# Kernel tuning notes

Hardware: AMD Instinct MI355X
Metric: run time of the kernel (lower is better)

The kernel has to match this reference:

```python
import jax, jax.numpy as jnp
import numpy as np

EPS = 1e-5
K = 20
NH = 16
SLOPE = 0.2

def leaky(x):
    return jnp.where(x >= 0, x, SLOPE * x)

def bn(x, g, b, axes):
    # training-mode batch norm (biased variance), channel axis = 1
    m = x.mean(axes, keepdims=True)
    v = x.var(axes, keepdims=True)
    shp = [1] * x.ndim
    shp[1] = -1
    return (x - m) / jnp.sqrt(v + EPS) * g.reshape(shp) + b.reshape(shp)

def efr(x, idx, w, k):
    # x: [B, C, N]; idx: flat global gather indices [B*N*k]; w: [C_out, 2C+1]
    B, C, N = x.shape
    xt = x.transpose(0, 2, 1).reshape(B * N, C)
    feature = xt[idx].reshape(B, N, k, C)            # gathered neighbors
    xc = xt.reshape(B, N, 1, C)
    fmean = feature.mean(-1, keepdims=True)          # [B,N,k,1]
    f = jnp.concatenate([feature - xc, fmean, jnp.broadcast_to(xc, feature.shape)], axis=3)
    return jnp.einsum('bnkc,oc->bonk', f, w)         # 1x1 conv -> [B,C_out,N,k]


def setup_inputs() -> dict:
    key = jax.random.key(0)
    ks = jax.random.split(key, 24)
    B, N = 8, 4096
    IN_CH, FEAT_CH, OUT_CH = 6, 64, 64
    d = {}
    d['points'] = jax.random.normal(ks[0], (B, IN_CH // 2, N), dtype=jnp.float32)
    d['feat'] = jax.random.normal(ks[1], (B, FEAT_CH // 2, N), dtype=jnp.float32)
    d['idx'] = jax.random.randint(ks[2], (B * N * K,), 0, B * N)
    s = 0.1
    d['w_efr_p'] = jax.random.normal(ks[3], (IN_CH, IN_CH + 1), dtype=jnp.float32) * s
    d['w_efr_f'] = jax.random.normal(ks[4], (FEAT_CH, FEAT_CH + 1), dtype=jnp.float32) * s
    d['w_q'] = jax.random.normal(ks[5], (FEAT_CH, FEAT_CH // 2), dtype=jnp.float32) * s
    d['g_q'] = jnp.ones((FEAT_CH,), jnp.float32)
    d['b_q'] = jnp.zeros((FEAT_CH,), jnp.float32)
    d['w_pos1'] = jax.random.normal(ks[6], (IN_CH, IN_CH // 2), dtype=jnp.float32) * s
    d['g_pos1'] = jnp.ones((IN_CH,), jnp.float32)
    d['b_pos1'] = jnp.zeros((IN_CH,), jnp.float32)
    d['w_pos2'] = jax.random.normal(ks[7], (FEAT_CH, IN_CH), dtype=jnp.float32) * s
    d['w_attn'] = jax.random.normal(ks[8], (NH * IN_CH, FEAT_CH), dtype=jnp.float32) * s
    d['g1'] = jnp.ones((NH,), jnp.float32)
    d['b1'] = jnp.zeros((NH,), jnp.float32)
    d['w_lin'] = jax.random.normal(ks[9], (OUT_CH, NH), dtype=jnp.float32) * s
    d['g_lin'] = jnp.ones((OUT_CH,), jnp.float32)
    d['b_lin'] = jnp.zeros((OUT_CH,), jnp.float32)
    d['w_res'] = jax.random.normal(ks[10], (OUT_CH, FEAT_CH), dtype=jnp.float32) * s
    d['g_res'] = jnp.ones((OUT_CH,), jnp.float32)
    d['b_res'] = jnp.zeros((OUT_CH,), jnp.float32)
    return d


def reference(points, feat, idx, w_efr_p, w_efr_f, w_q, g_q, b_q,
              w_pos1, g_pos1, b_pos1, w_pos2, w_attn, g1, b1,
              w_lin, g_lin, b_lin, w_res, g_res, b_res):
    B, _, N = points.shape
    knn_points = efr(points, idx, w_efr_p, K)   # [B,6,N,K]
    knn_feat = efr(feat, idx, w_efr_f, K)       # [B,64,N,K]
    x_q = leaky(bn(jnp.einsum('bcn,oc->bon', feat, w_q), g_q, b_q, (0, 2)))
    pos = leaky(bn(jnp.einsum('bcn,oc->bon', points, w_pos1), g_pos1, b_pos1, (0, 2)))
    pos = pos[:, :, :, None] - knn_points       # [B,6,N,K]
    pos = jnp.einsum('bcnk,oc->bonk', pos, w_pos2)  # [B,64,N,K]
    attn = x_q[:, :, :, None] - knn_feat + pos
    attn = jax.nn.softmax(attn / float(np.sqrt(knn_feat.shape[1])), axis=-1)
    attn = jnp.einsum('bcnk,oc->bonk', attn, w_attn)  # [B,NH*6,N,K]
    attn5 = attn.transpose(0, 2, 3, 1).reshape(B, N, K, NH, -1)  # [B,N,K,NH,6]
    y = jnp.einsum('bnkhc,bcnk->bhnk', attn5, knn_points)        # [B,NH,N,K]
    y = leaky(bn(y, g1, b1, (0, 2, 3)))
    y = bn(jnp.einsum('bcnk,oc->bonk', y, w_lin), g_lin, b_lin, (0, 2, 3))
    res = bn(jnp.einsum('bcnk,oc->bonk', knn_feat, w_res), g_res, b_res, (0, 2, 3))
    y = leaky(y + res)
    return y.max(axis=-1)                        # [B,64,N]
```

## Files before the change

kernel.cpp:

```cpp
#include <hip/hip_runtime.h>

#define KNN 20
#define NN 4096
#define NPTS 32768
#define PPW 8

using short8 = __attribute__((ext_vector_type(8))) short;
using f32x4v = __attribute__((ext_vector_type(4))) float;
using uint4v = __attribute__((ext_vector_type(4))) unsigned int;

__device__ __forceinline__ float lrelu(float x){ return x >= 0.f ? x : 0.2f*x; }
__device__ __forceinline__ unsigned short f2b(float x){
    union { float f; unsigned u; } v; v.f = x;
    unsigned r = v.u + 0x7FFFu + ((v.u >> 16) & 1u);
    return (unsigned short)(r >> 16);
}
__device__ __forceinline__ float b2f(unsigned h){
    union { unsigned u; float f; } v; v.u = h << 16; return v.f;
}
#define WSYNC() do { asm volatile("s_waitcnt lgkmcnt(0)" ::: "memory"); __builtin_amdgcn_sched_barrier(0); } while(0)

__device__ __forceinline__ int fslot(int fragi, int klocal, int gp){
    return fragi*1024 + (((klocal) + ((gp)<<4)) ^ ((gp)*5))*16;
}

__global__ void kprep(const float* __restrict__ weff, const float* __restrict__ wattn,
                      const float* __restrict__ wres, const float* __restrict__ wl,
                      unsigned short* __restrict__ packW, float* __restrict__ wdiff,
                      float* __restrict__ w32t, float* __restrict__ wrb,
                      float* __restrict__ rww)
{
    __shared__ float sres[4096];
    __shared__ float sweff[4160];
    __shared__ float scomb[2048];
    int t = threadIdx.x;
    for (int m=t; m<4096; m+=256) sres[m] = wres[m];
    for (int m=t; m<4160; m+=256) sweff[m] = weff[m];
    __syncthreads();
    for (int q=t;q<2048;q+=256){
        int c=q>>5, j=q&31;
        wdiff[q] = sweff[c*65+33+j]-sweff[c*65+j];
    }
    if (t<64) w32t[t] = sweff[t*65+32];
    for (int q=t;q<2048;q+=256){
        int o=q>>5, j=q&31;
        float a=0.f, b=0.f;
        for (int c=0;c<64;c++){
            float wr = sres[o*64+c];
            a += wr*sweff[c*65+j];
            b += wr*(sweff[c*65+33+j]-sweff[c*65+j]);
        }
        scomb[q]=a; wrb[q]=b;
    }
    if (t<64){
        float a=0.f;
        for (int c=0;c<64;c++) a += sres[t*64+c]*sweff[c*65+32];
        rww[t]=a;
    }
    __syncthreads();
    for (int q = t; q < 1536; q += 256){
        int f = q >> 6, l = q & 63;
        #pragma unroll
        for (int j=0;j<8;j++){
            int koff, n; float v;
            if (f < 4){ n = f*16 + (l&15); koff = 0;
                int k = koff + (j>=4?16:0) + 4*(l>>4) + (j&3);
                v = sweff[n*65 + k];
            } else if (f < 16){ int ff=f-4; n = (ff>>1)*16 + (l&15); koff = (ff&1)*32;
                int k = koff + (j>=4?16:0) + 4*(l>>4) + (j&3);
                v = wattn[n*64 + k];
            } else { int ff=f-16; n = (ff>>1)*16 + (l&15); koff = (ff&1)*32;
                int k = koff + (j>=4?16:0) + 4*(l>>4) + (j&3);
                v = sres[n*64 + k];
            }
            packW[(size_t)(f*64+l)*8 + j] = f2b(v);
        }
    }
    for (int q=t;q<512;q+=256){
        int f=q>>6, l=q&63;
        int nt = f&3; bool iswl = f>=4;
        #pragma unroll
        for (int j=0;j<8;j++){
            int kdim = (j>=4?16:0)+4*(l>>4)+(j&3);
            float v;
            if (!iswl) v = scomb[(nt*16+(l&15))*32 + kdim];
            else v = (kdim<16) ? wl[(nt*16+(l&15))*16 + kdim] : 0.f;
            packW[(size_t)((24+f)*64+l)*8+j] = f2b(v);
        }
    }
}

__global__ void __launch_bounds__(256) k0_prep(
    const float* __restrict__ pts, const float* __restrict__ feat,
    const float* __restrict__ wq, const float* __restrict__ wpos1,
    const float* __restrict__ wefp, const float* __restrict__ wdiff,
    const float* __restrict__ wrb,
    unsigned short* __restrict__ ft16, float* __restrict__ pt4,
    unsigned short* __restrict__ qp16, float* __restrict__ pp,
    unsigned short* __restrict__ base16, float* __restrict__ bpp,
    unsigned short* __restrict__ rb16,
    float* __restrict__ qsum, float* __restrict__ qsq,
    float* __restrict__ psum, float* __restrict__ psq)
{
    __shared__ float swq[2048];
    __shared__ float swd[2048];
    __shared__ float swr[2048];
    __shared__ float red[4][64], red2[4][64];
    int tid = threadIdx.x;
    for (int m=tid;m<2048;m+=256){ swq[m]=wq[m]; swd[m]=wdiff[m]; swr[m]=wrb[m]; }
    __syncthreads();
    int r = blockIdx.x*256 + tid;
    int b = r >> 12, n = r & 4095;
    float p0 = pts[((size_t)b*3+0)*NN+n];
    float p1 = pts[((size_t)b*3+1)*NN+n];
    float p2 = pts[((size_t)b*3+2)*NN+n];
    float pm = (p0+p1+p2)*(1.f/3.f);
    *(float4*)(pt4 + (size_t)r*4) = make_float4(p0,p1,p2,pm);
    float f[32];
    #pragma unroll
    for (int c=0;c<32;c++) f[c] = feat[((size_t)b*32+c)*NN+n];
    #pragma unroll
    for (int c=0;c<32;c+=2){
        unsigned pk = (unsigned)f2b(f[c]) | ((unsigned)f2b(f[c+1])<<16);
        *(unsigned*)(ft16 + (size_t)r*32 + c) = pk;
    }
    float q[64];
    for (int o=0;o<64;o++){
        float a=0.f;
        #pragma unroll
        for (int c=0;c<32;c++) a += swq[o*32+c]*f[c];
        q[o]=a;
    }
    for (int o=0;o<64;o+=2){
        unsigned pk = (unsigned)f2b(q[o]) | ((unsigned)f2b(q[o+1])<<16);
        *(unsigned*)(qp16 + (size_t)r*64 + o) = pk;
    }
    int lane = tid & 63, wvv = tid>>6;
    for (int o=0;o<64;o++){
        float s=q[o], s2=q[o]*q[o];
        for (int d=1; d<64; d<<=1){ s += __shfl_xor(s,d); s2 += __shfl_xor(s2,d); }
        if (lane==0){ red[wvv][o]=s; red2[wvv][o]=s2; }
    }
    __syncthreads();
    if (tid<64){
        atomicAdd(qsum+tid, red[0][tid]+red[1][tid]+red[2][tid]+red[3][tid]);
        atomicAdd(qsq+tid, red2[0][tid]+red2[1][tid]+red2[2][tid]+red2[3][tid]);
    }
    for (int o=0;o<64;o++){
        float a=0.f;
        #pragma unroll
        for (int c=0;c<32;c++) a += swd[o*32+c]*f[c];
        q[o]=a;
    }
    for (int o=0;o<64;o+=2){
        unsigned pk = (unsigned)f2b(q[o]) | ((unsigned)f2b(q[o+1])<<16);
        *(unsigned*)(base16 + (size_t)r*64 + o) = pk;
    }
    for (int o=0;o<64;o++){
        float a=0.f;
        #pragma unroll
        for (int c=0;c<32;c++) a += swr[o*32+c]*f[c];
        q[o]=a;
    }
    for (int o=0;o<64;o+=2){
        unsigned pk = (unsigned)f2b(q[o]) | ((unsigned)f2b(q[o+1])<<16);
        *(unsigned*)(rb16 + (size_t)r*64 + o) = pk;
    }
    float pr[8];
    #pragma unroll
    for (int o=0;o<6;o++) pr[o] = wpos1[o*3]*p0 + wpos1[o*3+1]*p1 + wpos1[o*3+2]*p2;
    pr[6]=0.f; pr[7]=0.f;
    *(float4*)(pp+(size_t)r*8)   = make_float4(pr[0],pr[1],pr[2],pr[3]);
    *(float4*)(pp+(size_t)r*8+4) = make_float4(pr[4],pr[5],pr[6],pr[7]);
    __syncthreads();
    for (int o=0;o<6;o++){
        float s=pr[o], s2=pr[o]*pr[o];
        for (int d=1;d<64;d<<=1){ s += __shfl_xor(s,d); s2 += __shfl_xor(s2,d); }
        if (lane==0){ red[wvv][o]=s; red2[wvv][o]=s2; }
    }
    __syncthreads();
    if (tid<6){
        atomicAdd(psum+tid, red[0][tid]+red[1][tid]+red[2][tid]+red[3][tid]);
        atomicAdd(psq+tid, red2[0][tid]+red2[1][tid]+red2[2][tid]+red2[3][tid]);
    }
    #pragma unroll
    for (int j=0;j<6;j++)
        bpp[(size_t)r*8+j] = p0*(wefp[j*7+4]-wefp[j*7]) + p1*(wefp[j*7+5]-wefp[j*7+1])
                           + p2*(wefp[j*7+6]-wefp[j*7+2]);
    bpp[(size_t)r*8+6]=0.f; bpp[(size_t)r*8+7]=0.f;
}

__global__ void k1_paramsA(
    const float* __restrict__ qsum, const float* __restrict__ qsq,
    const float* __restrict__ psum, const float* __restrict__ psq,
    const float* __restrict__ gq, const float* __restrict__ bq,
    const float* __restrict__ gp, const float* __restrict__ bp,
    float* __restrict__ bnq_a, float* __restrict__ bnq_c,
    float* __restrict__ bnp_a, float* __restrict__ bnp_c)
{
    int t = threadIdx.x;
    const float inv = 1.f/32768.f;
    if (t < 64){
        float m = qsum[t]*inv; float v = qsq[t]*inv - m*m;
        float a = gq[t]*rsqrtf(v + 1e-5f);
        bnq_a[t] = a; bnq_c[t] = bq[t] - m*a;
    }
    if (t < 6){
        float m = psum[t]*inv; float v = psq[t]*inv - m*m;
        float a = gp[t]*rsqrtf(v + 1e-5f);
        bnp_a[t] = a; bnp_c[t] = bp[t] - m*a;
    }
}

#define ARENA 10240
#define R1    0
#define R2    4096
#define SFM   8192
#define SSKP  8320
#define SIDX  8960
#define YST   9600

__global__ void __launch_bounds__(256, 3) k2_main(
    const unsigned short* __restrict__ ft16, const float* __restrict__ pt4,
    const unsigned short* __restrict__ qp16, const float* __restrict__ pp,
    const unsigned short* __restrict__ base16, const float* __restrict__ bpp,
    const int* __restrict__ idx,
    const float* __restrict__ wefp, const float* __restrict__ wpos2,
    const unsigned short* __restrict__ packW, const float* __restrict__ w32t,
    const float* __restrict__ bnq_a, const float* __restrict__ bnq_c,
    const float* __restrict__ bnp_a, const float* __restrict__ bnp_c,
    unsigned short* __restrict__ yv,
    float* __restrict__ yslot, float* __restrict__ rslot)
{
    __shared__ __align__(16) char smem_[4*ARENA];
    const int tid = threadIdx.x;
    const int l = tid & 63, wv = tid >> 6;
    const int lo = l & 15, g = l >> 4;
    char* S = smem_ + wv*ARENA;
    const int srd = (l ^ (g*5))*16;

    float w2r[4][6], w32r[4], bnqa[4], bnqc[4];
    #pragma unroll
    for (int nt=0;nt<4;nt++){
        #pragma unroll
        for (int j=0;j<6;j++) w2r[nt][j] = wpos2[(nt*16+lo)*6+j];
        w32r[nt] = w32t[nt*16+lo];
        bnqa[nt] = bnq_a[nt*16+lo];
        bnqc[nt] = bnq_c[nt*16+lo];
    }
    float bnpa[6], bnpc[6];
    #pragma unroll
    for (int j=0;j<6;j++){ bnpa[j]=bnp_a[j]; bnpc[j]=bnp_c[j]; }

    float ysum=0.f, ysq=0.f;
    float racc[4]={0.f,0.f,0.f,0.f}, rsqa[4]={0.f,0.f,0.f,0.f};

    const int rbase = blockIdx.x*(4*PPW) + wv*PPW;

    *(int*)(S+SIDX+l*4)        = idx[(size_t)rbase*KNN + l];
    *(int*)(S+SIDX+(64+l)*4)   = idx[(size_t)rbase*KNN + 64 + l];
    if (l < 32) *(int*)(S+SIDX+(128+l)*4) = idx[(size_t)rbase*KNN + 128 + l];
    WSYNC();

    for (int pi=0; pi<PPW; pi++){
        const size_t r = (size_t)(rbase + pi);
        float xqv[4], basev[4], sp[6];
        {
            int sb = pi*KNN*4;
            int i0 = *(const int*)(S+SIDX+sb+(l>>3)*4);
            int i1 = *(const int*)(S+SIDX+sb+(8+(l>>3))*4);
            uint2 ng0 = *(const uint2*)(ft16 + (size_t)i0*32 + (l&7)*4);
            uint2 ng1 = *(const uint2*)(ft16 + (size_t)i1*32 + (l&7)*4);
            uint2 ng2 = make_uint2(0u,0u);
            if (l < 32){
                int i2 = *(const int*)(S+SIDX+sb+(16+(l>>3))*4);
                ng2 = *(const uint2*)(ft16 + (size_t)i2*32 + (l&7)*4);
            }
            float4 ngp4 = make_float4(0,0,0,0);
            if (l < KNN){
                int ip = *(const int*)(S+SIDX+sb+l*4);
                ngp4 = *(const float4*)(pt4 + (size_t)ip*4);
            }
            float nbppr[6];
            if (l < KNN){
                #pragma unroll
                for (int j=0;j<6;j++) nbppr[j] = bpp[r*8+j];
            }
            float s0 = b2f(ng0.x&0xffffu)+b2f(ng0.x>>16)+b2f(ng0.y&0xffffu)+b2f(ng0.y>>16);
            float s1 = b2f(ng1.x&0xffffu)+b2f(ng1.x>>16)+b2f(ng1.y&0xffffu)+b2f(ng1.y>>16);
            float s2 = b2f(ng2.x&0xffffu)+b2f(ng2.x>>16)+b2f(ng2.y&0xffffu)+b2f(ng2.y>>16);
            s0 += __shfl_xor(s0,1); s0 += __shfl_xor(s0,2); s0 += __shfl_xor(s0,4);
            s1 += __shfl_xor(s1,1); s1 += __shfl_xor(s1,2); s1 += __shfl_xor(s1,4);
            s2 += __shfl_xor(s2,1); s2 += __shfl_xor(s2,2); s2 += __shfl_xor(s2,4);
            if ((l&7)==0){
                *(float*)(S+SFM+(l>>3)*4) = s0*(1.f/32.f);
                *(float*)(S+SFM+(8+(l>>3))*4) = s1*(1.f/32.f);
                if (l < 32) *(float*)(S+SFM+(16+(l>>3))*4) = s2*(1.f/32.f);
            }
            {
                int kk = l>>3, gp_ = l&3, jb = ((l>>2)&1)*8;
                *(uint2*)(S + R1 + fslot(0, kk, gp_) + jb) = ng0;
                *(uint2*)(S + R1 + fslot(0, 8+kk, gp_) + jb) = ng1;
                if (l < 32) *(uint2*)(S + R1 + fslot(1, kk, gp_) + jb) = ng2;
            }
            if (l < KNN){
                #pragma unroll
                for (int j=0;j<6;j++){
                    float v = nbppr[j] + wefp[j*7]*ngp4.x + wefp[j*7+1]*ngp4.y
                            + wefp[j*7+2]*ngp4.z + wefp[j*7+3]*ngp4.w;
                    *(float*)(S+SSKP+(l*8+j)*4) = v;
                }
            }
            #pragma unroll
            for (int nt=0;nt<4;nt++){
                xqv[nt] = lrelu(bnqa[nt]*b2f(qp16[r*64 + nt*16+lo]) + bnqc[nt]);
                basev[nt] = b2f(base16[r*64 + nt*16+lo]);
            }
            #pragma unroll
            for (int j=0;j<6;j++) sp[j] = lrelu(bnpa[j]*pp[r*8+j] + bnpc[j]);
            WSYNC();
        }

        f32x4v C1[2][4];
        #pragma unroll
        for (int mt=0;mt<2;mt++)
            #pragma unroll
            for (int nt=0;nt<4;nt++)
                #pragma unroll
                for (int i=0;i<4;i++) C1[mt][nt][i] = 0.f;
        short8 Af0 = *(const short8*)(S + R1 + 0*1024 + srd);
        short8 Af1 = *(const short8*)(S + R1 + 1*1024 + srd);
        #pragma unroll
        for (int nt=0;nt<4;nt++){
            short8 Bf = *(const short8*)(packW + (size_t)(nt*64 + l)*8);
            C1[0][nt] = __builtin_amdgcn_mfma_f32_16x16x32_bf16(Af0, Bf, C1[0][nt], 0, 0, 0);
            C1[1][nt] = __builtin_amdgcn_mfma_f32_16x16x32_bf16(Af1, Bf, C1[1][nt], 0, 0, 0);
        }
        #pragma unroll
        for (int mt=0;mt<2;mt++){
            #pragma unroll
            for (int i=0;i<4;i++){
                int k = mt*16 + g*4 + i;
                bool valid = (k < KNN);
                int kk = valid ? k : 0;
                float fmk = *(const float*)(S+SFM+kk*4);
                float sk[6];
                #pragma unroll
                for (int j=0;j<6;j++) sk[j] = *(const float*)(S+SSKP+(kk*8+j)*4);
                #pragma unroll
                for (int nt=0;nt<4;nt++){
                    float kf = C1[mt][nt][i] + basev[nt] + w32r[nt]*fmk;
                    if (valid){
                        int fa = fslot(mt*2+(nt>>1), g*4+i, lo>>2) + ((nt&1)*4 + (lo&3))*2;
                        *(unsigned short*)(S + R2 + fa) = f2b(kf);
                    }
                    float pos = 0.f;
                    #pragma unroll
                    for (int j=0;j<6;j++) pos += (sp[j]-sk[j])*w2r[nt][j];
                    C1[mt][nt][i] = valid ? (xqv[nt] - kf + pos)*0.125f : -1e30f;
                }
            }
        }
        #pragma unroll
        for (int nt=0;nt<4;nt++){
            float mx = -1e30f;
            #pragma unroll
            for (int mt=0;mt<2;mt++)
                #pragma unroll
                for (int i=0;i<4;i++) mx = fmaxf(mx, C1[mt][nt][i]);
            mx = fmaxf(mx, __shfl_xor(mx,16));
            mx = fmaxf(mx, __shfl_xor(mx,32));
            float sm = 0.f;
            #pragma unroll
            for (int mt=0;mt<2;mt++)
                #pragma unroll
                for (int i=0;i<4;i++){ float e = __expf(C1[mt][nt][i]-mx); C1[mt][nt][i]=e; sm += e; }
            sm += __shfl_xor(sm,16);
            sm += __shfl_xor(sm,32);
            float inv = 1.f/sm;
            #pragma unroll
            for (int mt=0;mt<2;mt++)
                #pragma unroll
                for (int i=0;i<4;i++){
                    int k = mt*16 + g*4 + i;
                    if (k < KNN){
                        int fa = fslot(mt*2+(nt>>1), g*4+i, lo>>2) + ((nt&1)*4 + (lo&3))*2;
                        *(unsigned short*)(S + R1 + fa) = f2b(C1[mt][nt][i]*inv);
                    }
                }
        }
        WSYNC();
        short8 Ak[2][2], Aa[2][2];
        #pragma unroll
        for (int mt=0;mt<2;mt++)
            #pragma unroll
            for (int s=0;s<2;s++){
                Ak[mt][s] = *(const short8*)(S + R2 + (mt*2+s)*1024 + srd);
                Aa[mt][s] = *(const short8*)(S + R1 + (mt*2+s)*1024 + srd);
            }
        f32x4v C3[2][4];
        #pragma unroll
        for (int mt=0;mt<2;mt++)
            #pragma unroll
            for (int nt=0;nt<4;nt++)
                #pragma unroll
                for (int i=0;i<4;i++) C3[mt][nt][i] = 0.f;
        #pragma unroll
        for (int nt=0;nt<4;nt++){
            #pragma unroll
            for (int s=0;s<2;s++){
                short8 Bf = *(const short8*)(packW + (size_t)((16+nt*2+s)*64 + l)*8);
                #pragma unroll
                for (int mt=0;mt<2;mt++)
                    C3[mt][nt] = __builtin_amdgcn_mfma_f32_16x16x32_bf16(Ak[mt][s], Bf, C3[mt][nt], 0, 0, 0);
            }
        }
        #pragma unroll
        for (int mt=0;mt<2;mt++)
            #pragma unroll
            for (int i=0;i<4;i++){
                int k = mt*16 + g*4 + i;
                if (k < KNN){
                    #pragma unroll
                    for (int nt=0;nt<4;nt++){
                        float v = C3[mt][nt][i];
                        racc[nt] += v; rsqa[nt] += v*v;
                    }
                }
            }
        f32x4v C2[2][6];
        #pragma unroll
        for (int mt=0;mt<2;mt++)
            #pragma unroll
            for (int nt=0;nt<6;nt++)
                #pragma unroll
                for (int i=0;i<4;i++) C2[mt][nt][i] = 0.f;
        #pragma unroll
        for (int nt=0;nt<6;nt++){
            #pragma unroll
            for (int s=0;s<2;s++){
                short8 Bf = *(const short8*)(packW + (size_t)((4+nt*2+s)*64 + l)*8);
                #pragma unroll
                for (int mt=0;mt<2;mt++)
                    C2[mt][nt] = __builtin_amdgcn_mfma_f32_16x16x32_bf16(Aa[mt][s], Bf, C2[mt][nt], 0, 0, 0);
            }
        }
        #pragma unroll
        for (int mt=0;mt<2;mt++)
            #pragma unroll
            for (int nt=0;nt<6;nt++)
                #pragma unroll
                for (int i=0;i<4;i++){
                    int k = mt*16 + g*4 + i;
                    if (k < KNN)
                        *(unsigned short*)(S + R2 + k*200 + (nt*16+lo)*2) = f2b(C2[mt][nt][i]);
                }
        WSYNC();
        #pragma unroll
        for (int it=0; it<5; it++){
            int kq = it*4 + g;
            const char* row = S + R2 + kq*200 + lo*12;
            unsigned d0 = *(const unsigned*)(row);
            unsigned d1 = *(const unsigned*)(row+4);
            unsigned d2 = *(const unsigned*)(row+8);
            float yval = b2f(d0&0xffffu) * (*(const float*)(S+SSKP+(kq*8+0)*4))
                       + b2f(d0>>16)    * (*(const float*)(S+SSKP+(kq*8+1)*4))
                       + b2f(d1&0xffffu)* (*(const float*)(S+SSKP+(kq*8+2)*4))
                       + b2f(d1>>16)    * (*(const float*)(S+SSKP+(kq*8+3)*4))
                       + b2f(d2&0xffffu)* (*(const float*)(S+SSKP+(kq*8+4)*4))
                       + b2f(d2>>16)    * (*(const float*)(S+SSKP+(kq*8+5)*4));
            *(unsigned short*)(S + YST + kq*32 + lo*2) = f2b(yval);
            ysum += yval; ysq += yval*yval;
        }
        WSYNC();
        if (l < 40){
            uint4v v = *(const uint4v*)(S + YST + l*16);
            *(uint4v*)((char*)yv + r*640 + l*16) = v;
        }
    }
    ysum += __shfl_xor(ysum,16); ysum += __shfl_xor(ysum,32);
    ysq  += __shfl_xor(ysq,16);  ysq  += __shfl_xor(ysq,32);
    #pragma unroll
    for (int nt=0;nt<4;nt++){
        racc[nt] += __shfl_xor(racc[nt],16); racc[nt] += __shfl_xor(racc[nt],32);
        rsqa[nt] += __shfl_xor(rsqa[nt],16); rsqa[nt] += __shfl_xor(rsqa[nt],32);
    }
    int slot = (blockIdx.x*4 + wv) & 63;
    if (l < 16){
        atomicAdd(yslot + slot*32 + l, ysum);
        #pragma unroll
        for (int nt=0;nt<4;nt++) atomicAdd(rslot + slot*128 + nt*16 + l, racc[nt]);
    } else if (l < 32){
        atomicAdd(yslot + slot*32 + 16 + lo, ysq);
        #pragma unroll
        for (int nt=0;nt<4;nt++) atomicAdd(rslot + slot*128 + 64 + nt*16 + lo, rsqa[nt]);
    }
}

__global__ void k3_paramsB(
    const float* __restrict__ yslot, const float* __restrict__ rslot,
    const float* __restrict__ g1, const float* __restrict__ b1,
    const float* __restrict__ gr, const float* __restrict__ br,
    float* __restrict__ bn1_a, float* __restrict__ bn1_c,
    float* __restrict__ bnr_a, float* __restrict__ bnr_c)
{
    __shared__ float sy[32];
    __shared__ float sr[128];
    int t = threadIdx.x;
    float s1 = 0.f;
    if (t < 32){ for (int i=0;i<64;i++) s1 += yslot[(size_t)i*32+t]; }
    float s2 = 0.f;
    for (int i=0;i<64;i++) s2 += rslot[(size_t)i*128+t];
    if (t < 32) sy[t] = s1;
    sr[t] = s2;
    __syncthreads();
    const float inv = 1.f/655360.f;
    if (t < 16){
        float m = sy[t]*inv; float v = sy[16+t]*inv - m*m;
        float a = g1[t]*rsqrtf(v + 1e-5f);
        bn1_a[t] = a; bn1_c[t] = b1[t] - m*a;
    }
    if (t < 64){
        float m = sr[t]*inv; float v = sr[64+t]*inv - m*m;
        float a = gr[t]*rsqrtf(v + 1e-5f);
        bnr_a[t] = a; bnr_c[t] = br[t] - m*a;
    }
}

__global__ void __launch_bounds__(256) k4_linstats(
    const unsigned short* __restrict__ yv,
    const float* __restrict__ bn1_a, const float* __restrict__ bn1_c,
    float* __restrict__ Mslot, float* __restrict__ Sslot)
{
    __shared__ __align__(16) char lds[4*1024];
    const int tid = threadIdx.x, l = tid & 63, wvv = tid >> 6;
    const int lo = l & 15, g = l >> 4;
    char* L = lds + wvv*1024;
    const int h0 = (l&1)*8;
    float a8[8], c8[8];
    #pragma unroll
    for (int j=0;j<8;j++){ a8[j]=bn1_a[h0+j]; c8[j]=bn1_c[h0+j]; }
    short8 ones;
    #pragma unroll
    for (int j=0;j<8;j++) ones[j] = (short)0x3F80;
    f32x4v Macc, Sacc;
    #pragma unroll
    for (int i=0;i<4;i++){ Macc[i]=0.f; Sacc[i]=0.f; }
    const int waveid = blockIdx.x*4 + wvv;
    for (int it=0; it<5; it++){
        size_t s0 = ((size_t)waveid*5 + it)*32;
        uint4 v = *(const uint4*)(yv + s0*16 + l*8);
        unsigned short e0 = v.x&0xffffu, e1 = v.x>>16, e2 = v.y&0xffffu, e3 = v.y>>16;
        unsigned short e4 = v.z&0xffffu, e5 = v.z>>16, e6 = v.w&0xffffu, e7 = v.w>>16;
        float y0 = lrelu(a8[0]*b2f(e0)+c8[0]), y1 = lrelu(a8[1]*b2f(e1)+c8[1]);
        float y2_ = lrelu(a8[2]*b2f(e2)+c8[2]), y3 = lrelu(a8[3]*b2f(e3)+c8[3]);
        float y4 = lrelu(a8[4]*b2f(e4)+c8[4]), y5 = lrelu(a8[5]*b2f(e5)+c8[5]);
        float y6 = lrelu(a8[6]*b2f(e6)+c8[6]), y7 = lrelu(a8[7]*b2f(e7)+c8[7]);
        uint4 o;
        o.x = (unsigned)f2b(y0) | ((unsigned)f2b(y1)<<16);
        o.y = (unsigned)f2b(y2_)| ((unsigned)f2b(y3)<<16);
        o.z = (unsigned)f2b(y4) | ((unsigned)f2b(y5)<<16);
        o.w = (unsigned)f2b(y6) | ((unsigned)f2b(y7)<<16);
        *(uint4*)(L + l*16) = o;
        WSYNC();
        short8 Af;
        #pragma unroll
        for (int j=0;j<8;j++){
            int s = 4*g + (j&3) + ((j>=4)?16:0);
            Af[j] = *(const short*)(L + s*32 + lo*2);
        }
        WSYNC();
        Macc = __builtin_amdgcn_mfma_f32_16x16x32_bf16(Af, Af, Macc, 0, 0, 0);
        Sacc = __builtin_amdgcn_mfma_f32_16x16x32_bf16(ones, Af, Sacc, 0, 0, 0);
    }
    float* Ms = Mslot + (size_t)(waveid&15)*256;
    #pragma unroll
    for (int i=0;i<4;i++) atomicAdd(Ms + (g*4+i)*16 + lo, Macc[i]);
    if (l < 16) atomicAdd(Sslot + (size_t)(waveid&15)*16 + lo, Sacc[0]);
}

__global__ void k5_paramsC(
    const float* __restrict__ Mslot, const float* __restrict__ Sslot,
    const float* __restrict__ wl,
    const float* __restrict__ gl, const float* __restrict__ bl,
    float* __restrict__ bnl_a, float* __restrict__ bnl_c)
{
    __shared__ float Ms[256], Ss[16];
    int t = threadIdx.x;
    float m = 0.f;
    for (int i=0;i<16;i++) m += Mslot[(size_t)i*256+t];
    Ms[t] = m;
    if (t < 16){
        float s = 0.f;
        for (int i=0;i<16;i++) s += Sslot[(size_t)i*16+t];
        Ss[t] = s;
    }
    __syncthreads();
    if (t < 64){
        float w[16];
        #pragma unroll
        for (int h=0;h<16;h++) w[h] = wl[t*16+h];
        float lsum = 0.f;
        #pragma unroll
        for (int h=0;h<16;h++) lsum += w[h]*Ss[h];
        float lsq = 0.f;
        for (int h1=0;h1<16;h1++){
            float acc = 0.f;
            #pragma unroll
            for (int h2=0;h2<16;h2++) acc += Ms[h1*16+h2]*w[h2];
            lsq += w[h1]*acc;
        }
        const float inv = 1.f/655360.f;
        float mean = lsum*inv; float var = lsq*inv - mean*mean;
        float a = gl[t]*rsqrtf(var + 1e-5f);
        bnl_a[t] = a; bnl_c[t] = bl[t] - mean*a;
    }
}

#define ARENA6 2848
#define SFM6 2048
#define SIDX6 2176

__global__ void __launch_bounds__(256) k6_final(
    const unsigned short* __restrict__ ft16, const unsigned short* __restrict__ yv,
    const int* __restrict__ idx, const unsigned short* __restrict__ rb16,
    const unsigned short* __restrict__ packW, const float* __restrict__ rww,
    const float* __restrict__ bn1_a, const float* __restrict__ bn1_c,
    const float* __restrict__ bnl_a, const float* __restrict__ bnl_c,
    const float* __restrict__ bnr_a, const float* __restrict__ bnr_c,
    float* __restrict__ out)
{
    __shared__ __align__(16) char smem_[4*ARENA6];
    __shared__ float sval[64*36];
    const int tid = threadIdx.x;
    const int l = tid & 63, wv = tid >> 6;
    const int lo = l & 15, g = l >> 4;
    char* S = smem_ + wv*ARENA6;
    const int srd = (l ^ (g*5))*16;

    short8 Bc[4], Bl[4];
    #pragma unroll
    for (int nt=0;nt<4;nt++){
        Bc[nt] = *(const short8*)(packW + (size_t)((24+nt)*64+l)*8);
        Bl[nt] = *(const short8*)(packW + (size_t)((28+nt)*64+l)*8);
    }
    float4 b1a = *(const float4*)(bn1_a + 4*g);
    float4 b1c = *(const float4*)(bn1_c + 4*g);
    float la[4], lc[4], ra[4], rc[4], rwv[4];
    #pragma unroll
    for (int nt=0;nt<4;nt++){
        int o = nt*16+lo;
        la[nt]=bnl_a[o]; lc[nt]=bnl_c[o]; ra[nt]=bnr_a[o]; rc[nt]=bnr_c[o]; rwv[nt]=rww[o];
    }
    const int rbase = blockIdx.x*32 + wv*8;
    *(int*)(S+SIDX6+l*4)      = idx[(size_t)rbase*KNN + l];
    *(int*)(S+SIDX6+(64+l)*4) = idx[(size_t)rbase*KNN + 64 + l];
    if (l < 32) *(int*)(S+SIDX6+(128+l)*4) = idx[(size_t)rbase*KNN + 128 + l];
    WSYNC();

    for (int pi=0; pi<8; pi++){
        size_t rr = (size_t)(rbase + pi);
        short8 AlyA, AlyB; float rbv[4];
        {
            int sb = pi*KNN*4;
            int i0 = *(const int*)(S+SIDX6+sb+(l>>3)*4);
            int i1 = *(const int*)(S+SIDX6+sb+(8+(l>>3))*4);
            uint2 ng0 = *(const uint2*)(ft16 + (size_t)i0*32 + (l&7)*4);
            uint2 ng1 = *(const uint2*)(ft16 + (size_t)i1*32 + (l&7)*4);
            uint2 ng2 = make_uint2(0u,0u);
            if (l < 32){
                int i2 = *(const int*)(S+SIDX6+sb+(16+(l>>3))*4);
                ng2 = *(const uint2*)(ft16 + (size_t)i2*32 + (l&7)*4);
            }
            uint2 ylo_ = *(const uint2*)(yv + rr*320 + (l&15)*16 + g*4);
            uint2 yhi_ = make_uint2(0u,0u);
            if (lo < 4) yhi_ = *(const uint2*)(yv + rr*320 + (16+(l&15))*16 + g*4);
            unsigned short rbr[4];
            #pragma unroll
            for (int nt=0;nt<4;nt++) rbr[nt] = rb16[rr*64 + nt*16+lo];

            float s0 = b2f(ng0.x&0xffffu)+b2f(ng0.x>>16)+b2f(ng0.y&0xffffu)+b2f(ng0.y>>16);
            float s1 = b2f(ng1.x&0xffffu)+b2f(ng1.x>>16)+b2f(ng1.y&0xffffu)+b2f(ng1.y>>16);
            float s2 = b2f(ng2.x&0xffffu)+b2f(ng2.x>>16)+b2f(ng2.y&0xffffu)+b2f(ng2.y>>16);
            s0 += __shfl_xor(s0,1); s0 += __shfl_xor(s0,2); s0 += __shfl_xor(s0,4);
            s1 += __shfl_xor(s1,1); s1 += __shfl_xor(s1,2); s1 += __shfl_xor(s1,4);
            s2 += __shfl_xor(s2,1); s2 += __shfl_xor(s2,2); s2 += __shfl_xor(s2,4);
            if ((l&7)==0){
                *(float*)(S+SFM6+(l>>3)*4) = s0*(1.f/32.f);
                *(float*)(S+SFM6+(8+(l>>3))*4) = s1*(1.f/32.f);
                if (l < 32) *(float*)(S+SFM6+(16+(l>>3))*4) = s2*(1.f/32.f);
            }
            {
                int kk = l>>3, gp_ = l&3, jb = ((l>>2)&1)*8;
                *(uint2*)(S + fslot(0, kk, gp_) + jb) = ng0;
                *(uint2*)(S + fslot(0, 8+kk, gp_) + jb) = ng1;
                if (l < 32) *(uint2*)(S + fslot(1, kk, gp_) + jb) = ng2;
            }
            float t0 = lrelu(b1a.x*b2f(ylo_.x&0xffffu)+b1c.x);
            float t1 = lrelu(b1a.y*b2f(ylo_.x>>16)+b1c.y);
            float t2 = lrelu(b1a.z*b2f(ylo_.y&0xffffu)+b1c.z);
            float t3 = lrelu(b1a.w*b2f(ylo_.y>>16)+b1c.w);
            AlyA[0]=(short)f2b(t0); AlyA[1]=(short)f2b(t1); AlyA[2]=(short)f2b(t2); AlyA[3]=(short)f2b(t3);
            AlyA[4]=0; AlyA[5]=0; AlyA[6]=0; AlyA[7]=0;
            t0 = lrelu(b1a.x*b2f(yhi_.x&0xffffu)+b1c.x);
            t1 = lrelu(b1a.y*b2f(yhi_.x>>16)+b1c.y);
            t2 = lrelu(b1a.z*b2f(yhi_.y&0xffffu)+b1c.z);
            t3 = lrelu(b1a.w*b2f(yhi_.y>>16)+b1c.w);
            AlyB[0]=(short)f2b(t0); AlyB[1]=(short)f2b(t1); AlyB[2]=(short)f2b(t2); AlyB[3]=(short)f2b(t3);
            AlyB[4]=0; AlyB[5]=0; AlyB[6]=0; AlyB[7]=0;
            #pragma unroll
            for (int nt=0;nt<4;nt++) rbv[nt] = b2f(rbr[nt]);
            WSYNC();
        }

        short8 Af0 = *(const short8*)(S + 0*1024 + srd);
        short8 Af1 = *(const short8*)(S + 1*1024 + srd);
        f32x4v Crv[2][4], Clv[2][4];
        #pragma unroll
        for (int mt=0;mt<2;mt++)
            #pragma unroll
            for (int nt=0;nt<4;nt++)
                #pragma unroll
                for (int i=0;i<4;i++){ Crv[mt][nt][i]=0.f; Clv[mt][nt][i]=0.f; }
        #pragma unroll
        for (int nt=0;nt<4;nt++){
            Crv[0][nt] = __builtin_amdgcn_mfma_f32_16x16x32_bf16(Af0, Bc[nt], Crv[0][nt], 0, 0, 0);
            Crv[1][nt] = __builtin_amdgcn_mfma_f32_16x16x32_bf16(Af1, Bc[nt], Crv[1][nt], 0, 0, 0);
            Clv[0][nt] = __builtin_amdgcn_mfma_f32_16x16x32_bf16(AlyA, Bl[nt], Clv[0][nt], 0, 0, 0);
            Clv[1][nt] = __builtin_amdgcn_mfma_f32_16x16x32_bf16(AlyB, Bl[nt], Clv[1][nt], 0, 0, 0);
        }
        float vmax[4] = {-1e30f,-1e30f,-1e30f,-1e30f};
        #pragma unroll
        for (int mt=0;mt<2;mt++)
            #pragma unroll
            for (int i=0;i<4;i++){
                int k = mt*16 + g*4 + i;
                if (k < KNN){
                    float fmk = *(const float*)(S+SFM6+k*4);
                    #pragma unroll
                    for (int nt=0;nt<4;nt++){
                        float rv = Crv[mt][nt][i] + rbv[nt] + rwv[nt]*fmk;
                        float lv = Clv[mt][nt][i];
                        float val = lrelu(la[nt]*lv + lc[nt] + ra[nt]*rv + rc[nt]);
                        vmax[nt] = fmaxf(vmax[nt], val);
                    }
                }
            }
        #pragma unroll
        for (int nt=0;nt<4;nt++){
            vmax[nt] = fmaxf(vmax[nt], __shfl_xor(vmax[nt],16));
            vmax[nt] = fmaxf(vmax[nt], __shfl_xor(vmax[nt],32));
        }
        if (l < 16){
            #pragma unroll
            for (int nt=0;nt<4;nt++)
                sval[(nt*16+lo)*36 + wv*8 + pi] = vmax[nt];
        }
        WSYNC();
    }
    __syncthreads();
    {
        int o = tid >> 2, seg = tid & 3;
        float4 v0 = *(const float4*)(sval + o*36 + seg*8);
        float4 v1 = *(const float4*)(sval + o*36 + seg*8 + 4);
        size_t base = ((size_t)(blockIdx.x>>7)*64 + o)*NN + (blockIdx.x&127)*32 + seg*8;
        *(float4*)(out + base) = v0;
        *(float4*)(out + base + 4) = v1;
    }
}

extern "C" void kernel_launch(void* const* d_in, const int* in_sizes, int n_in,
                              void* d_out, int out_size, void* d_ws, size_t ws_size,
                              hipStream_t stream)
{
    const float* pts   = (const float*)d_in[0];
    const float* feat  = (const float*)d_in[1];
    const int*   idx   = (const int*)d_in[2];
    const float* wefp  = (const float*)d_in[3];
    const float* weff  = (const float*)d_in[4];
    const float* wq    = (const float*)d_in[5];
    const float* gq    = (const float*)d_in[6];
    const float* bq    = (const float*)d_in[7];
    const float* wpos1 = (const float*)d_in[8];
    const float* gp    = (const float*)d_in[9];
    const float* bp    = (const float*)d_in[10];
    const float* wpos2 = (const float*)d_in[11];
    const float* wattn = (const float*)d_in[12];
    const float* g1    = (const float*)d_in[13];
    const float* b1    = (const float*)d_in[14];
    const float* wl    = (const float*)d_in[15];
    const float* gl    = (const float*)d_in[16];
    const float* bl    = (const float*)d_in[17];
    const float* wres  = (const float*)d_in[18];
    const float* gr    = (const float*)d_in[19];
    const float* br    = (const float*)d_in[20];
    float* out = (float*)d_out;

    char* ws = (char*)d_ws;
    size_t o_ft16 = 0;
    size_t o_pt4  = o_ft16 + (size_t)NPTS*64;
    size_t o_qp16 = o_pt4  + (size_t)NPTS*16;
    size_t o_pp   = o_qp16 + (size_t)NPTS*128;
    size_t o_b16  = o_pp   + (size_t)NPTS*32;
    size_t o_bpp  = o_b16  + (size_t)NPTS*128;
    size_t o_rb16 = o_bpp  + (size_t)NPTS*32;
    size_t o_packW= o_rb16 + (size_t)NPTS*128;
    size_t o_wdiff= o_packW + 32*512*2;
    size_t o_wrb  = o_wdiff + 2048*4;
    size_t o_rw   = o_wrb   + 2048*4;
    size_t o_w32  = o_rw    + 64*4;
    size_t o_st   = o_w32   + 64*4;
    size_t o_qsum  = o_st;
    size_t o_qsq   = o_qsum + 64*4;
    size_t o_psum  = o_qsq  + 64*4;
    size_t o_psq   = o_psum + 8*4;
    size_t o_yslot = o_psq  + 8*4;
    size_t o_rslot = o_yslot + (size_t)64*32*4;
    size_t o_mslot = o_rslot + (size_t)64*128*4;
    size_t o_sslot = o_mslot + (size_t)16*256*4;
    size_t zero_bytes = (o_sslot + (size_t)16*16*4) - o_st;
    size_t o_par   = o_st + zero_bytes;
    size_t o_bnq_a = o_par;
    size_t o_bnq_c = o_bnq_a + 64*4;
    size_t o_bnp_a = o_bnq_c + 64*4;
    size_t o_bnp_c = o_bnp_a + 8*4;
    size_t o_bn1_a = o_bnp_c + 8*4;
    size_t o_bn1_c = o_bn1_a + 16*4;
    size_t o_bnl_a = o_bn1_c + 16*4;
    size_t o_bnl_c = o_bnl_a + 64*4;
    size_t o_bnr_a = o_bnl_c + 64*4;
    size_t o_bnr_c = o_bnr_a + 64*4;
    size_t o_yv = (o_bnr_c + 64*4 + 255) & ~(size_t)255;

    unsigned short* ft16 = (unsigned short*)(ws + o_ft16);
    float* pt4  = (float*)(ws + o_pt4);
    unsigned short* qp16 = (unsigned short*)(ws + o_qp16);
    float* ppb  = (float*)(ws + o_pp);
    unsigned short* b16p = (unsigned short*)(ws + o_b16);
    float* bppb = (float*)(ws + o_bpp);
    unsigned short* rb16 = (unsigned short*)(ws + o_rb16);
    unsigned short* packW = (unsigned short*)(ws + o_packW);
    float* wdiff= (float*)(ws + o_wdiff);
    float* wrb  = (float*)(ws + o_wrb);
    float* rww  = (float*)(ws + o_rw);
    float* w32t = (float*)(ws + o_w32);
    float* qsum = (float*)(ws + o_qsum);
    float* qsq  = (float*)(ws + o_qsq);
    float* psum = (float*)(ws + o_psum);
    float* psq  = (float*)(ws + o_psq);
    float* yslot= (float*)(ws + o_yslot);
    float* rslot= (float*)(ws + o_rslot);
    float* Mslot= (float*)(ws + o_mslot);
    float* Sslot= (float*)(ws + o_sslot);
    float* bnq_a= (float*)(ws + o_bnq_a);
    float* bnq_c= (float*)(ws + o_bnq_c);
    float* bnp_a= (float*)(ws + o_bnp_a);
    float* bnp_c= (float*)(ws + o_bnp_c);
    float* bn1_a= (float*)(ws + o_bn1_a);
    float* bn1_c= (float*)(ws + o_bn1_c);
    float* bnl_a= (float*)(ws + o_bnl_a);
    float* bnl_c= (float*)(ws + o_bnl_c);
    float* bnr_a= (float*)(ws + o_bnr_a);
    float* bnr_c= (float*)(ws + o_bnr_c);
    unsigned short* yvp = (unsigned short*)(ws + o_yv);

    (void)hipMemsetAsync(ws + o_st, 0, zero_bytes, stream);

    kprep<<<1, 256, 0, stream>>>(weff, wattn, wres, wl, packW, wdiff, w32t, wrb, rww);
    k0_prep<<<128, 256, 0, stream>>>(pts, feat, wq, wpos1, wefp, wdiff, wrb,
                                     ft16, pt4, qp16, ppb, b16p, bppb, rb16,
                                     qsum, qsq, psum, psq);
    k1_paramsA<<<1, 64, 0, stream>>>(qsum, qsq, psum, psq, gq, bq, gp, bp,
                                     bnq_a, bnq_c, bnp_a, bnp_c);
    k2_main<<<NPTS/(4*PPW), 256, 0, stream>>>(ft16, pt4, qp16, ppb, b16p, bppb, idx,
                                     wefp, wpos2, packW, w32t,
                                     bnq_a, bnq_c, bnp_a, bnp_c,
                                     yvp, yslot, rslot);
    k3_paramsB<<<1, 128, 0, stream>>>(yslot, rslot, g1, b1, gr, br,
                                      bn1_a, bn1_c, bnr_a, bnr_c);
    k4_linstats<<<1024, 256, 0, stream>>>(yvp, bn1_a, bn1_c, Mslot, Sslot);
    k5_paramsC<<<1, 256, 0, stream>>>(Mslot, Sslot, wl, gl, bl, bnl_a, bnl_c);
    k6_final<<<1024, 256, 0, stream>>>(ft16, yvp, idx, rb16, packW, rww,
                                       bn1_a, bn1_c, bnl_a, bnl_c, bnr_a, bnr_c, out);
}
```

Measured before the change: 480.5 us.

## Interleave bf16 features and points into 128-byte gather records; read idx directly

Packs each point's bf16 features (64 bytes) and its float4 point/mean into a single 128-byte record, so a neighbour's feature and coordinate gathers fall in the same cache line. The per-wave LDS staging of neighbour indices is removed from both k2_main and k6_final; indices are now read straight from global memory. This shrinks the LDS arenas, which could allow higher occupancy. The cost is extra global idx loads per point and a doubled stride for feature records.

After: 508.6 us. +5.9%, slower.

```diff
diff --git a/kernel.cpp b/kernel.cpp
--- a/kernel.cpp
+++ b/kernel.cpp
@@ -95,7 +95,7 @@
     const float* __restrict__ wq, const float* __restrict__ wpos1,
     const float* __restrict__ wefp, const float* __restrict__ wdiff,
     const float* __restrict__ wrb,
-    unsigned short* __restrict__ ft16, float* __restrict__ pt4,
+    char* __restrict__ grec,
     unsigned short* __restrict__ qp16, float* __restrict__ pp,
     unsigned short* __restrict__ base16, float* __restrict__ bpp,
     unsigned short* __restrict__ rb16,
@@ -115,14 +115,14 @@
     float p1 = pts[((size_t)b*3+1)*NN+n];
     float p2 = pts[((size_t)b*3+2)*NN+n];
     float pm = (p0+p1+p2)*(1.f/3.f);
-    *(float4*)(pt4 + (size_t)r*4) = make_float4(p0,p1,p2,pm);
+    *(float4*)(grec + (size_t)r*128 + 64) = make_float4(p0,p1,p2,pm);
     float f[32];
     #pragma unroll
     for (int c=0;c<32;c++) f[c] = feat[((size_t)b*32+c)*NN+n];
     #pragma unroll
     for (int c=0;c<32;c+=2){
         unsigned pk = (unsigned)f2b(f[c]) | ((unsigned)f2b(f[c+1])<<16);
-        *(unsigned*)(ft16 + (size_t)r*32 + c) = pk;
+        *(unsigned*)(grec + (size_t)r*128 + c*2) = pk;
     }
     float q[64];
     for (int o=0;o<64;o++){
@@ -212,16 +212,15 @@
     }
 }
 
-#define ARENA 10240
+#define ARENA 8960
 #define R1    0
 #define R2    4096
 #define SFM   8192
 #define SSKP  8320
-#define SIDX  8960
-#define YST   9600
+#define YST   0
 
 __global__ void __launch_bounds__(256, 3) k2_main(
-    const unsigned short* __restrict__ ft16, const float* __restrict__ pt4,
+    const char* __restrict__ grec,
     const unsigned short* __restrict__ qp16, const float* __restrict__ pp,
     const unsigned short* __restrict__ base16, const float* __restrict__ bpp,
     const int* __restrict__ idx,
@@ -257,29 +256,23 @@
 
     const int rbase = blockIdx.x*(4*PPW) + wv*PPW;
 
-    *(int*)(S+SIDX+l*4)        = idx[(size_t)rbase*KNN + l];
-    *(int*)(S+SIDX+(64+l)*4)   = idx[(size_t)rbase*KNN + 64 + l];
-    if (l < 32) *(int*)(S+SIDX+(128+l)*4) = idx[(size_t)rbase*KNN + 128 + l];
-    WSYNC();
-
     for (int pi=0; pi<PPW; pi++){
         const size_t r = (size_t)(rbase + pi);
         float xqv[4], basev[4], sp[6];
         {
-            int sb = pi*KNN*4;
-            int i0 = *(const int*)(S+SIDX+sb+(l>>3)*4);
-            int i1 = *(const int*)(S+SIDX+sb+(8+(l>>3))*4);
-            uint2 ng0 = *(const uint2*)(ft16 + (size_t)i0*32 + (l&7)*4);
-            uint2 ng1 = *(const uint2*)(ft16 + (size_t)i1*32 + (l&7)*4);
+            int i0 = idx[r*KNN + (l>>3)];
+            int i1 = idx[r*KNN + 8 + (l>>3)];
+            uint2 ng0 = *(const uint2*)(grec + (size_t)i0*128 + (l&7)*8);
+            uint2 ng1 = *(const uint2*)(grec + (size_t)i1*128 + (l&7)*8);
             uint2 ng2 = make_uint2(0u,0u);
             if (l < 32){
-                int i2 = *(const int*)(S+SIDX+sb+(16+(l>>3))*4);
-                ng2 = *(const uint2*)(ft16 + (size_t)i2*32 + (l&7)*4);
+                int i2 = idx[r*KNN + 16 + (l>>3)];
+                ng2 = *(const uint2*)(grec + (size_t)i2*128 + (l&7)*8);
             }
             float4 ngp4 = make_float4(0,0,0,0);
             if (l < KNN){
-                int ip = *(const int*)(S+SIDX+sb+l*4);
-                ngp4 = *(const float4*)(pt4 + (size_t)ip*4);
+                int ip = idx[r*KNN + l];
+                ngp4 = *(const float4*)(grec + (size_t)ip*128 + 64);
             }
             float nbppr[6];
             if (l < KNN){
@@ -617,12 +610,11 @@
     }
 }
 
-#define ARENA6 2848
+#define ARENA6 2176
 #define SFM6 2048
-#define SIDX6 2176
 
 __global__ void __launch_bounds__(256) k6_final(
-    const unsigned short* __restrict__ ft16, const unsigned short* __restrict__ yv,
+    const char* __restrict__ grec, const unsigned short* __restrict__ yv,
     const int* __restrict__ idx, const unsigned short* __restrict__ rb16,
     const unsigned short* __restrict__ packW, const float* __restrict__ rww,
     const float* __restrict__ bn1_a, const float* __restrict__ bn1_c,
@@ -653,24 +645,19 @@
         la[nt]=bnl_a[o]; lc[nt]=bnl_c[o]; ra[nt]=bnr_a[o]; rc[nt]=bnr_c[o]; rwv[nt]=rww[o];
     }
     const int rbase = blockIdx.x*32 + wv*8;
-    *(int*)(S+SIDX6+l*4)      = idx[(size_t)rbase*KNN + l];
-    *(int*)(S+SIDX6+(64+l)*4) = idx[(size_t)rbase*KNN + 64 + l];
-    if (l < 32) *(int*)(S+SIDX6+(128+l)*4) = idx[(size_t)rbase*KNN + 128 + l];
-    WSYNC();
 
     for (int pi=0; pi<8; pi++){
         size_t rr = (size_t)(rbase + pi);
         short8 AlyA, AlyB; float rbv[4];
         {
-            int sb = pi*KNN*4;
-            int i0 = *(const int*)(S+SIDX6+sb+(l>>3)*4);
-            int i1 = *(const int*)(S+SIDX6+sb+(8+(l>>3))*4);
-            uint2 ng0 = *(const uint2*)(ft16 + (size_t)i0*32 + (l&7)*4);
-            uint2 ng1 = *(const uint2*)(ft16 + (size_t)i1*32 + (l&7)*4);
+            int i0 = idx[rr*KNN + (l>>3)];
+            int i1 = idx[rr*KNN + 8 + (l>>3)];
+            uint2 ng0 = *(const uint2*)(grec + (size_t)i0*128 + (l&7)*8);
+            uint2 ng1 = *(const uint2*)(grec + (size_t)i1*128 + (l&7)*8);
             uint2 ng2 = make_uint2(0u,0u);
             if (l < 32){
-                int i2 = *(const int*)(S+SIDX6+sb+(16+(l>>3))*4);
-                ng2 = *(const uint2*)(ft16 + (size_t)i2*32 + (l&7)*4);
+                int i2 = idx[rr*KNN + 16 + (l>>3)];
+                ng2 = *(const uint2*)(grec + (size_t)i2*128 + (l&7)*8);
             }
             uint2 ylo_ = *(const uint2*)(yv + rr*320 + (l&15)*16 + g*4);
             uint2 yhi_ = make_uint2(0u,0u);
@@ -797,9 +784,8 @@
     float* out = (float*)d_out;
 
     char* ws = (char*)d_ws;
-    size_t o_ft16 = 0;
-    size_t o_pt4  = o_ft16 + (size_t)NPTS*64;
-    size_t o_qp16 = o_pt4  + (size_t)NPTS*16;
+    size_t o_grec = 0;
+    size_t o_qp16 = o_grec + (size_t)NPTS*128;
     size_t o_pp   = o_qp16 + (size_t)NPTS*128;
     size_t o_b16  = o_pp   + (size_t)NPTS*32;
     size_t o_bpp  = o_b16  + (size_t)NPTS*128;
@@ -832,8 +818,7 @@
     size_t o_bnr_c = o_bnr_a + 64*4;
     size_t o_yv = (o_bnr_c + 64*4 + 255) & ~(size_t)255;
 
-    unsigned short* ft16 = (unsigned short*)(ws + o_ft16);
-    float* pt4  = (float*)(ws + o_pt4);
+    char* grec = ws + o_grec;
     unsigned short* qp16 = (unsigned short*)(ws + o_qp16);
     float* ppb  = (float*)(ws + o_pp);
     unsigned short* b16p = (unsigned short*)(ws + o_b16);
@@ -868,11 +853,11 @@
 
     kprep<<<1, 256, 0, stream>>>(weff, wattn, wres, wl, packW, wdiff, w32t, wrb, rww);
     k0_prep<<<128, 256, 0, stream>>>(pts, feat, wq, wpos1, wefp, wdiff, wrb,
-                                     ft16, pt4, qp16, ppb, b16p, bppb, rb16,
+                                     grec, qp16, ppb, b16p, bppb, rb16,
                                      qsum, qsq, psum, psq);
     k1_paramsA<<<1, 64, 0, stream>>>(qsum, qsq, psum, psq, gq, bq, gp, bp,
                                      bnq_a, bnq_c, bnp_a, bnp_c);
-    k2_main<<<NPTS/(4*PPW), 256, 0, stream>>>(ft16, pt4, qp16, ppb, b16p, bppb, idx,
+    k2_main<<<NPTS/(4*PPW), 256, 0, stream>>>(grec, qp16, ppb, b16p, bppb, idx,
                                      wefp, wpos2, packW, w32t,
                                      bnq_a, bnq_c, bnp_a, bnp_c,
                                      yvp, yslot, rslot);
@@ -880,6 +865,6 @@
                                       bn1_a, bn1_c, bnr_a, bnr_c);
     k4_linstats<<<1024, 256, 0, stream>>>(yvp, bn1_a, bn1_c, Mslot, Sslot);
     k5_paramsC<<<1, 256, 0, stream>>>(Mslot, Sslot, wl, gl, bl, bnl_a, bnl_c);
-    k6_final<<<1024, 256, 0, stream>>>(ft16, yvp, idx, rb16, packW, rww,
+    k6_final<<<1024, 256, 0, stream>>>(grec, yvp, idx, rb16, packW, rww,
                                        bn1_a, bn1_c, bnl_a, bnl_c, bnr_a, bnr_c, out);
 }
```

## Software-prefetch next point's neighbor gathers in k2 and drop LDS index staging

Applied to the files above, without the earlier changes.

In the main kernel, the gathers of neighbor features, point data and bias for the next point are issued from global memory into registers while the current point's MFMA post-processing runs. This replaces the per-wave LDS staging of the neighbor index list. The LDS arena shrinks in both k2 and k6, and k6 now reads indices directly from global memory. The aim is to hide gather latency and allow higher occupancy, at the cost of more live registers, which could cause spills under the launch bound of 3.

Result: slower. 537.0 us (+11.8%).

```diff
diff --git a/kernel.cpp b/kernel.cpp
--- a/kernel.cpp
+++ b/kernel.cpp
@@ -212,13 +212,12 @@
     }
 }
 
-#define ARENA 10240
+#define ARENA 8960
 #define R1    0
 #define R2    4096
 #define SFM   8192
 #define SSKP  8320
-#define SIDX  8960
-#define YST   9600
+#define YST   0
 
 __global__ void __launch_bounds__(256, 3) k2_main(
     const unsigned short* __restrict__ ft16, const float* __restrict__ pt4,
@@ -257,35 +256,33 @@
 
     const int rbase = blockIdx.x*(4*PPW) + wv*PPW;
 
-    *(int*)(S+SIDX+l*4)        = idx[(size_t)rbase*KNN + l];
-    *(int*)(S+SIDX+(64+l)*4)   = idx[(size_t)rbase*KNN + 64 + l];
-    if (l < 32) *(int*)(S+SIDX+(128+l)*4) = idx[(size_t)rbase*KNN + 128 + l];
-    WSYNC();
+    uint2 png0, png1, png2;
+    float4 pngp4;
+    float pbpp[6];
+
+#define PREFETCH(pi_) { \
+    size_t rn = (size_t)(rbase + (pi_)); \
+    int i0 = idx[rn*KNN + (l>>3)]; \
+    int i1 = idx[rn*KNN + 8 + (l>>3)]; \
+    png0 = *(const uint2*)(ft16 + (size_t)i0*32 + (l&7)*4); \
+    png1 = *(const uint2*)(ft16 + (size_t)i1*32 + (l&7)*4); \
+    png2 = make_uint2(0u,0u); pngp4 = make_float4(0,0,0,0); \
+    if (l < 32){ int i2 = idx[rn*KNN + 16 + (l>>3)]; \
+                 png2 = *(const uint2*)(ft16 + (size_t)i2*32 + (l&7)*4); } \
+    if (l < KNN){ int ip = idx[rn*KNN + l]; \
+                  pngp4 = *(const float4*)(pt4 + (size_t)ip*4); \
+                  _Pragma("unroll") for (int j=0;j<6;j++) pbpp[j] = bpp[rn*8+j]; } \
+    __builtin_amdgcn_sched_barrier(0); \
+}
+
+    PREFETCH(0);
 
     for (int pi=0; pi<PPW; pi++){
         const size_t r = (size_t)(rbase + pi);
         float xqv[4], basev[4], sp[6];
         {
-            int sb = pi*KNN*4;
-            int i0 = *(const int*)(S+SIDX+sb+(l>>3)*4);
-            int i1 = *(const int*)(S+SIDX+sb+(8+(l>>3))*4);
-            uint2 ng0 = *(const uint2*)(ft16 + (size_t)i0*32 + (l&7)*4);
-            uint2 ng1 = *(const uint2*)(ft16 + (size_t)i1*32 + (l&7)*4);
-            uint2 ng2 = make_uint2(0u,0u);
-            if (l < 32){
-                int i2 = *(const int*)(S+SIDX+sb+(16+(l>>3))*4);
-                ng2 = *(const uint2*)(ft16 + (size_t)i2*32 + (l&7)*4);
-            }
-            float4 ngp4 = make_float4(0,0,0,0);
-            if (l < KNN){
-                int ip = *(const int*)(S+SIDX+sb+l*4);
-                ngp4 = *(const float4*)(pt4 + (size_t)ip*4);
-            }
-            float nbppr[6];
-            if (l < KNN){
-                #pragma unroll
-                for (int j=0;j<6;j++) nbppr[j] = bpp[r*8+j];
-            }
+            uint2 ng0 = png0, ng1 = png1, ng2 = png2;
+            float4 ngp4 = pngp4;
             float s0 = b2f(ng0.x&0xffffu)+b2f(ng0.x>>16)+b2f(ng0.y&0xffffu)+b2f(ng0.y>>16);
             float s1 = b2f(ng1.x&0xffffu)+b2f(ng1.x>>16)+b2f(ng1.y&0xffffu)+b2f(ng1.y>>16);
             float s2 = b2f(ng2.x&0xffffu)+b2f(ng2.x>>16)+b2f(ng2.y&0xffffu)+b2f(ng2.y>>16);
@@ -306,7 +303,7 @@
             if (l < KNN){
                 #pragma unroll
                 for (int j=0;j<6;j++){
-                    float v = nbppr[j] + wefp[j*7]*ngp4.x + wefp[j*7+1]*ngp4.y
+                    float v = pbpp[j] + wefp[j*7]*ngp4.x + wefp[j*7+1]*ngp4.y
                             + wefp[j*7+2]*ngp4.z + wefp[j*7+3]*ngp4.w;
                     *(float*)(S+SSKP+(l*8+j)*4) = v;
                 }
@@ -456,6 +453,7 @@
                         *(unsigned short*)(S + R2 + k*200 + (nt*16+lo)*2) = f2b(C2[mt][nt][i]);
                 }
         WSYNC();
+        if (pi < PPW-1) PREFETCH(pi+1);
         #pragma unroll
         for (int it=0; it<5; it++){
             int kq = it*4 + g;
@@ -495,6 +493,7 @@
         #pragma unroll
         for (int nt=0;nt<4;nt++) atomicAdd(rslot + slot*128 + 64 + nt*16 + lo, rsqa[nt]);
     }
+#undef PREFETCH
 }
 
 __global__ void k3_paramsB(
@@ -617,12 +616,12 @@
     }
 }
 
-#define ARENA6 2848
+#define ARENA6 2176
 #define SFM6 2048
-#define SIDX6 2176
 
 __global__ void __launch_bounds__(256) k6_final(
-    const unsigned short* __restrict__ ft16, const unsigned short* __restrict__ yv,
+    const unsigned short* __restrict__ ft16, const float* __restrict__ pt4unused,
+    const unsigned short* __restrict__ yv,
     const int* __restrict__ idx, const unsigned short* __restrict__ rb16,
     const unsigned short* __restrict__ packW, const float* __restrict__ rww,
     const float* __restrict__ bn1_a, const float* __restrict__ bn1_c,
@@ -653,23 +652,18 @@
         la[nt]=bnl_a[o]; lc[nt]=bnl_c[o]; ra[nt]=bnr_a[o]; rc[nt]=bnr_c[o]; rwv[nt]=rww[o];
     }
     const int rbase = blockIdx.x*32 + wv*8;
-    *(int*)(S+SIDX6+l*4)      = idx[(size_t)rbase*KNN + l];
-    *(int*)(S+SIDX6+(64+l)*4) = idx[(size_t)rbase*KNN + 64 + l];
-    if (l < 32) *(int*)(S+SIDX6+(128+l)*4) = idx[(size_t)rbase*KNN + 128 + l];
-    WSYNC();
 
     for (int pi=0; pi<8; pi++){
         size_t rr = (size_t)(rbase + pi);
         short8 AlyA, AlyB; float rbv[4];
         {
-            int sb = pi*KNN*4;
-            int i0 = *(const int*)(S+SIDX6+sb+(l>>3)*4);
-            int i1 = *(const int*)(S+SIDX6+sb+(8+(l>>3))*4);
+            int i0 = idx[rr*KNN + (l>>3)];
+            int i1 = idx[rr*KNN + 8 + (l>>3)];
             uint2 ng0 = *(const uint2*)(ft16 + (size_t)i0*32 + (l&7)*4);
             uint2 ng1 = *(const uint2*)(ft16 + (size_t)i1*32 + (l&7)*4);
             uint2 ng2 = make_uint2(0u,0u);
             if (l < 32){
-                int i2 = *(const int*)(S+SIDX6+sb+(16+(l>>3))*4);
+                int i2 = idx[rr*KNN + 16 + (l>>3)];
                 ng2 = *(const uint2*)(ft16 + (size_t)i2*32 + (l&7)*4);
             }
             uint2 ylo_ = *(const uint2*)(yv + rr*320 + (l&15)*16 + g*4);
@@ -880,6 +874,6 @@
                                       bn1_a, bn1_c, bnr_a, bnr_c);
     k4_linstats<<<1024, 256, 0, stream>>>(yvp, bn1_a, bn1_c, Mslot, Sslot);
     k5_paramsC<<<1, 256, 0, stream>>>(Mslot, Sslot, wl, gl, bl, bnl_a, bnl_c);
-    k6_final<<<1024, 256, 0, stream>>>(ft16, yvp, idx, rb16, packW, rww,
+    k6_final<<<1024, 256, 0, stream>>>(ft16, pt4, yvp, idx, rb16, packW, rww,
                                        bn1_a, bn1_c, bnl_a, bnl_c, bnr_a, bnr_c, out);
 }
```
